# Optimization experiments

Hardware: AMD Instinct MI355X
Metric: run time of the kernel (lower is better)

The kernel has to match this reference:

```python
import jax, jax.numpy as jnp
import numpy as np

N_NODES = 50000
N_EDGES = 800000
N_GRAPHS = 2000
N_PAIRS = 4096
IN_CH = 64
EMB = 128
HID = 256
OUT = 1


def gcn_conv(x, edge_index, W, b):
    # PyG GCNConv: h = x @ W^T, then D^{-1/2}(A+I)D^{-1/2} h + b
    h = x @ W.T                                  # [N, out]
    row, col = edge_index[0], edge_index[1]
    ones = jnp.ones((edge_index.shape[1],), h.dtype)
    deg = jax.ops.segment_sum(ones, col, num_segments=N_NODES) + 1.0  # self-loop
    dinv = jax.lax.rsqrt(deg)
    norm = dinv[row] * dinv[col]                 # [E]
    agg = jax.ops.segment_sum(h[row] * norm[:, None], col, num_segments=N_NODES)
    agg = agg + h * (1.0 / deg)[:, None]         # self-loop term (dinv[i]^2)
    return agg + b


def setup_inputs() -> dict:
    key = jax.random.key(0)
    ks = jax.random.split(key, 10)
    x = jax.random.normal(ks[0], (N_NODES, IN_CH), jnp.float32)
    edge_index = jax.random.randint(ks[1], (2, N_EDGES), 0, N_NODES, jnp.int64)
    batch = jnp.sort(jax.random.randint(ks[2], (N_NODES,), 0, N_GRAPHS, jnp.int64))
    drug_drug_batch = jax.random.randint(ks[3], (2, N_PAIRS), 0, N_GRAPHS, jnp.int64)

    def xavier(k, shape):
        fan_out, fan_in = shape
        lim = jnp.sqrt(6.0 / (fan_in + fan_out))
        return jax.random.uniform(k, shape, jnp.float32, -lim, lim)

    return {
        "x": x, "edge_index": edge_index, "batch": batch,
        "drug_drug_batch": drug_drug_batch,
        "conv1_w": xavier(ks[4], (EMB, IN_CH)), "conv1_b": jnp.zeros((EMB,), jnp.float32),
        "conv2_w": xavier(ks[5], (EMB, EMB)), "conv2_b": jnp.zeros((EMB,), jnp.float32),
        "reg1_w": xavier(ks[6], (HID, 2 * EMB)), "reg1_b": jnp.zeros((HID,), jnp.float32),
        "reg2_w": xavier(ks[7], (OUT, HID)), "reg2_b": jnp.zeros((OUT,), jnp.float32),
    }


def reference(x, edge_index, batch, drug_drug_batch,
              conv1_w, conv1_b, conv2_w, conv2_b,
              reg1_w, reg1_b, reg2_w, reg2_b):
    h = jax.nn.relu(gcn_conv(x, edge_index, conv1_w, conv1_b))
    h = jax.nn.relu(gcn_conv(h, edge_index, conv2_w, conv2_b))

    # scatter_mean readout over graphs
    gsum = jax.ops.segment_sum(h, batch, num_segments=N_GRAPHS)
    cnt = jax.ops.segment_sum(jnp.ones((N_NODES,), h.dtype), batch, num_segments=N_GRAPHS)
    graph_embeds = gsum / jnp.maximum(cnt, 1.0)[:, None]

    # quantize drug ids to dense graph indices (np.digitize on unique+1, as in source)
    dd = np.asarray(drug_drug_batch)
    bins = np.unique(dd.flatten()) + 1
    q = jnp.asarray(np.digitize(dd, bins))       # [2, P]

    pairs = jnp.concatenate([graph_embeds[q[0]], graph_embeds[q[1]]], axis=1)  # [P, 2*EMB]
    out = jax.nn.relu(pairs @ reg1_w.T + reg1_b)
    return out @ reg2_w.T + reg2_b
```

## Files before the change

kernel.cpp:

```cpp
#include <hip/hip_runtime.h>

#define N_NODES  50000
#define N_PAD    50048
#define N_EDGES  800000
#define N_GRAPHS 2000
#define N_PAIRS  4096
#define IN_CH    64
#define EMB      128
#define HID      256
#define PPB      16
#define DPAD     16
#define GROB     1563

__device__ inline int wave_incl_scan(int x, int lane) {
    #pragma unroll
    for (int off = 1; off < 64; off <<= 1) {
        int y = __shfl_up(x, off, 64);
        if (lane >= off) x += y;
    }
    return x;
}

__global__ void k_zero(float4* __restrict__ p, int n4) {
    int i = blockIdx.x * 256 + threadIdx.x;
    if (i < n4) p[i] = make_float4(0.f, 0.f, 0.f, 0.f);
}

__global__ void k_pre(const int* __restrict__ col, const int* __restrict__ batch,
                      const float* __restrict__ w1, const float* __restrict__ w2,
                      int* __restrict__ deg, int* __restrict__ pos_e, int* __restrict__ cnt,
                      float* __restrict__ wt1, float* __restrict__ wt2,
                      const int* __restrict__ dd, int* __restrict__ rankx,
                      float4* __restrict__ gsum4) {
    int b = blockIdx.x, t = threadIdx.x;
    if (b < N_EDGES / 256) {
        int e = b * 256 + t;
        int c = col[e];
        pos_e[e] = atomicAdd(&deg[c * DPAD], 1);
        if (e < N_NODES) atomicAdd(&cnt[batch[e]], 1);
        if (e < EMB * IN_CH) {
            int j = e / IN_CH, k = e % IN_CH;
            wt1[k * EMB + j] = w1[e];
        } else if (e < EMB * IN_CH + EMB * EMB) {
            int q = e - EMB * IN_CH;
            int j = q / EMB, k = q % EMB;
            wt2[k * EMB + j] = w2[q];
        }
    } else if (b == N_EDGES / 256) {
        __shared__ int pres[N_GRAPHS];
        __shared__ int ws2[4];
        __shared__ int carry;
        int lane = t & 63, wid = t >> 6;
        for (int i = t; i < N_GRAPHS; i += 256) pres[i] = 0;
        __syncthreads();
        for (int i = t; i < 2 * N_PAIRS; i += 256) pres[dd[i]] = 1;
        if (t == 0) carry = 0;
        __syncthreads();
        for (int base = 0; base < N_GRAPHS; base += 256) {
            int i = base + t;
            int v = (i < N_GRAPHS) ? pres[i] : 0;
            int x = wave_incl_scan(v, lane);
            if (lane == 63) ws2[wid] = x;
            __syncthreads();
            int add = carry;
            for (int w = 0; w < wid; ++w) add += ws2[w];
            if (i < N_GRAPHS) rankx[i] = x - v + add;
            __syncthreads();
            if (t == 255) carry = add + x;
            __syncthreads();
        }
    } else {
        int i = (b - N_EDGES / 256 - 1) * 256 + t;
        for (int k = i; k < N_GRAPHS * EMB / 4; k += 4096)
            gsum4[k] = make_float4(0.f, 0.f, 0.f, 0.f);
    }
}

__global__ void k_scan1(const int* __restrict__ in, int* __restrict__ part, int n) {
    __shared__ int ws[4];
    int i = blockIdx.x * 256 + threadIdx.x;
    int lane = threadIdx.x & 63, wid = threadIdx.x >> 6;
    int v = (i < n) ? in[i * DPAD] : 0;
    int x = wave_incl_scan(v, lane);
    if (lane == 63) ws[wid] = x;
    __syncthreads();
    if (threadIdx.x == 0) part[blockIdx.x] = ws[0] + ws[1] + ws[2] + ws[3];
}

__global__ void k_scan3d(const int* __restrict__ in, const int* __restrict__ part,
                         int* __restrict__ off, float* __restrict__ dinv) {
    __shared__ int ws[4];
    __shared__ int psum[4];
    int t = threadIdx.x;
    int lane = t & 63, wid = t >> 6;
    int pp = 0;
    for (int w = t; w < (int)blockIdx.x; w += 256) pp += part[w];
    #pragma unroll
    for (int o = 32; o > 0; o >>= 1) pp += __shfl_down(pp, o, 64);
    if (lane == 0) psum[wid] = pp;
    int i = blockIdx.x * 256 + t;
    int v = (i < N_NODES) ? in[i * DPAD] : 0;
    int x = wave_incl_scan(v, lane);
    if (lane == 63) ws[wid] = x;
    __syncthreads();
    int add = psum[0] + psum[1] + psum[2] + psum[3];
    for (int w = 0; w < wid; ++w) add += ws[w];
    if (i < N_NODES) {
        off[i] = x - v + add;
        dinv[i] = 1.0f / sqrtf((float)(v + 1));
    }
    if (i == 0) off[N_NODES] = N_EDGES;
}

__global__ void k_fill_scale(const int* __restrict__ row, const int* __restrict__ col,
                             const int* __restrict__ pos_e, const int* __restrict__ off,
                             int* __restrict__ csr_row,
                             const float4* __restrict__ x, const float* __restrict__ dinv,
                             float4* __restrict__ xs) {
    int idx = blockIdx.x * 256 + threadIdx.x;
    if (idx < N_EDGES) {
        int c = col[idx];
        int p = pos_e[idx];
        csr_row[off[c] + p] = row[idx];
    } else {
        int i = idx - N_EDGES;
        int n = i >> 4;
        float d = dinv[n];
        float4 v = x[i];
        v.x *= d; v.y *= d; v.z *= d; v.w *= d;
        xs[i] = v;
    }
}

__device__ inline void f4add(float4& a, const float4 b) {
    a.x += b.x; a.y += b.y; a.z += b.z; a.w += b.w;
}

__global__ __launch_bounds__(256) void k_conv1f(
        const float4* __restrict__ xs, const int* __restrict__ csr_row,
        const int* __restrict__ off, const float* __restrict__ dinv,
        const float* __restrict__ w1t, const float* __restrict__ b1,
        float* __restrict__ h1s) {
    __shared__ __align__(16) float a_lds[32 * IN_CH];
    int t = threadIdx.x;
    int base = blockIdx.x * 32;
    {
        int c4l = t & 7;
        int nl = t >> 3;
        int n = base + nl;
        int s = 0, e = 0;
        float dn = 0.f;
        if (n < N_NODES) { s = off[n]; e = off[n + 1]; dn = dinv[n]; }
        #pragma unroll
        for (int g = 0; g < 2; ++g) {
            int c4 = c4l + g * 8;
            float4 acc = make_float4(0.f, 0.f, 0.f, 0.f);
            if (n < N_NODES) {
                acc = xs[n * 16 + c4];
                int i = s;
                for (; i + 8 <= e; i += 8) {
                    int r0 = csr_row[i + 0], r1 = csr_row[i + 1], r2 = csr_row[i + 2], r3 = csr_row[i + 3];
                    int r4 = csr_row[i + 4], r5 = csr_row[i + 5], r6 = csr_row[i + 6], r7 = csr_row[i + 7];
                    float4 a0 = xs[r0 * 16 + c4], a1 = xs[r1 * 16 + c4];
                    float4 a2 = xs[r2 * 16 + c4], a3 = xs[r3 * 16 + c4];
                    float4 a4 = xs[r4 * 16 + c4], a5 = xs[r5 * 16 + c4];
                    float4 a6 = xs[r6 * 16 + c4], a7 = xs[r7 * 16 + c4];
                    f4add(a0, a1); f4add(a2, a3); f4add(a4, a5); f4add(a6, a7);
                    f4add(a0, a2); f4add(a4, a6);
                    f4add(a0, a4);
                    f4add(acc, a0);
                }
                for (; i < e; ++i) {
                    float4 a = xs[csr_row[i] * 16 + c4];
                    f4add(acc, a);
                }
                acc.x *= dn; acc.y *= dn; acc.z *= dn; acc.w *= dn;
            }
            *reinterpret_cast<float4*>(&a_lds[nl * IN_CH + c4 * 4]) = acc;
        }
    }
    __syncthreads();
    {
        int cq = (t & 31) << 2;
        int rg = t >> 5;
        float4 acc[4];
        #pragma unroll
        for (int r = 0; r < 4; ++r) acc[r] = make_float4(0.f, 0.f, 0.f, 0.f);
        #pragma unroll 2
        for (int k = 0; k < IN_CH; k += 4) {
            float4 w0 = *reinterpret_cast<const float4*>(&w1t[(k + 0) * EMB + cq]);
            float4 w1 = *reinterpret_cast<const float4*>(&w1t[(k + 1) * EMB + cq]);
            float4 w2 = *reinterpret_cast<const float4*>(&w1t[(k + 2) * EMB + cq]);
            float4 w3 = *reinterpret_cast<const float4*>(&w1t[(k + 3) * EMB + cq]);
            #pragma unroll
            for (int r = 0; r < 4; ++r) {
                float4 a = *reinterpret_cast<const float4*>(&a_lds[(rg * 4 + r) * IN_CH + k]);
                acc[r].x = fmaf(a.x, w0.x, fmaf(a.y, w1.x, fmaf(a.z, w2.x, fmaf(a.w, w3.x, acc[r].x))));
                acc[r].y = fmaf(a.x, w0.y, fmaf(a.y, w1.y, fmaf(a.z, w2.y, fmaf(a.w, w3.y, acc[r].y))));
                acc[r].z = fmaf(a.x, w0.z, fmaf(a.y, w1.z, fmaf(a.z, w2.z, fmaf(a.w, w3.z, acc[r].z))));
                acc[r].w = fmaf(a.x, w0.w, fmaf(a.y, w1.w, fmaf(a.z, w2.w, fmaf(a.w, w3.w, acc[r].w))));
            }
        }
        float4 bv = *reinterpret_cast<const float4*>(&b1[cq]);
        #pragma unroll
        for (int r = 0; r < 4; ++r) {
            int row = base + rg * 4 + r;
            if (row < N_NODES) {
                float4 v = acc[r];
                v.x += bv.x; v.y += bv.y; v.z += bv.z; v.w += bv.w;
                float sc = dinv[row];
                v.x = fmaxf(v.x, 0.f) * sc; v.y = fmaxf(v.y, 0.f) * sc;
                v.z = fmaxf(v.z, 0.f) * sc; v.w = fmaxf(v.w, 0.f) * sc;
                *reinterpret_cast<float4*>(&h1s[(size_t)row * EMB + cq]) = v;
            }
        }
    }
}

template <int K>
__global__ void k_gemmv5(const float* __restrict__ A, const float* __restrict__ Wt,
                         float* __restrict__ out) {
    __shared__ __align__(16) float a_lds[64 * K];
    int t = threadIdx.x;
    {
        const float4* Ag = reinterpret_cast<const float4*>(A + (size_t)blockIdx.x * 64 * K);
        float4* Al = reinterpret_cast<float4*>(a_lds);
        constexpr int NV = (64 * K) / (4 * 256);
        #pragma unroll
        for (int i = 0; i < NV; ++i) Al[t + i * 256] = Ag[t + i * 256];
    }
    __syncthreads();
    int cq = (t & 31) << 2;
    int rg = t >> 5;
    float4 acc[8];
    #pragma unroll
    for (int r = 0; r < 8; ++r) acc[r] = make_float4(0.f, 0.f, 0.f, 0.f);
    #pragma unroll 2
    for (int k = 0; k < K; k += 4) {
        float4 w0 = *reinterpret_cast<const float4*>(&Wt[(k + 0) * EMB + cq]);
        float4 w1 = *reinterpret_cast<const float4*>(&Wt[(k + 1) * EMB + cq]);
        float4 w2 = *reinterpret_cast<const float4*>(&Wt[(k + 2) * EMB + cq]);
        float4 w3 = *reinterpret_cast<const float4*>(&Wt[(k + 3) * EMB + cq]);
        #pragma unroll
        for (int r = 0; r < 8; ++r) {
            float4 a = *reinterpret_cast<const float4*>(&a_lds[(rg * 8 + r) * K + k]);
            acc[r].x = fmaf(a.x, w0.x, fmaf(a.y, w1.x, fmaf(a.z, w2.x, fmaf(a.w, w3.x, acc[r].x))));
            acc[r].y = fmaf(a.x, w0.y, fmaf(a.y, w1.y, fmaf(a.z, w2.y, fmaf(a.w, w3.y, acc[r].y))));
            acc[r].z = fmaf(a.x, w0.z, fmaf(a.y, w1.z, fmaf(a.z, w2.z, fmaf(a.w, w3.z, acc[r].z))));
            acc[r].w = fmaf(a.x, w0.w, fmaf(a.y, w1.w, fmaf(a.z, w2.w, fmaf(a.w, w3.w, acc[r].w))));
        }
    }
    int row0 = blockIdx.x * 64 + rg * 8;
    #pragma unroll
    for (int r = 0; r < 8; ++r) {
        int row = row0 + r;
        if (row < N_NODES) {
            *reinterpret_cast<float4*>(&out[(size_t)row * EMB + cq]) = acc[r];
        }
    }
}

__global__ void k_gro(const float4* __restrict__ t2, const int* __restrict__ csr_row,
                      const int* __restrict__ off, const float* __restrict__ dinv,
                      const float* __restrict__ bias, const int* __restrict__ batch,
                      float* __restrict__ gsum) {
    __shared__ __align__(16) float hb[32][64];
    __shared__ int bg[32];
    int t = threadIdx.x;
    int bid = blockIdx.x;
    int half = (bid >= GROB) ? 1 : 0;
    int n0 = (half ? bid - GROB : bid) * 32;
    int local = t >> 3;
    int c4l = t & 7;
    int n = n0 + local;
    if (t < 32) bg[t] = (n0 + t < N_NODES) ? batch[n0 + t] : -1;
    int s = 0, e = 0;
    float dn = 0.f;
    bool valid = (n < N_NODES);
    if (valid) { s = off[n]; e = off[n + 1]; dn = dinv[n]; }
    #pragma unroll
    for (int g = 0; g < 2; ++g) {
        int cidx = half * 16 + g * 8 + c4l;
        float4 acc = make_float4(0.f, 0.f, 0.f, 0.f);
        if (valid) {
            acc = t2[(size_t)n * 32 + cidx];
            int i = s;
            for (; i + 8 <= e; i += 8) {
                int r0 = csr_row[i + 0], r1 = csr_row[i + 1], r2 = csr_row[i + 2], r3 = csr_row[i + 3];
                int r4 = csr_row[i + 4], r5 = csr_row[i + 5], r6 = csr_row[i + 6], r7 = csr_row[i + 7];
                float4 a0 = t2[(size_t)r0 * 32 + cidx], a1 = t2[(size_t)r1 * 32 + cidx];
                float4 a2 = t2[(size_t)r2 * 32 + cidx], a3 = t2[(size_t)r3 * 32 + cidx];
                float4 a4 = t2[(size_t)r4 * 32 + cidx], a5 = t2[(size_t)r5 * 32 + cidx];
                float4 a6 = t2[(size_t)r6 * 32 + cidx], a7 = t2[(size_t)r7 * 32 + cidx];
                f4add(a0, a1); f4add(a2, a3); f4add(a4, a5); f4add(a6, a7);
                f4add(a0, a2); f4add(a4, a6);
                f4add(a0, a4);
                f4add(acc, a0);
            }
            for (; i < e; ++i) {
                float4 a = t2[(size_t)csr_row[i] * 32 + cidx];
                f4add(acc, a);
            }
            float4 b = reinterpret_cast<const float4*>(bias)[cidx];
            acc.x = fmaxf(fmaf(acc.x, dn, b.x), 0.f);
            acc.y = fmaxf(fmaf(acc.y, dn, b.y), 0.f);
            acc.z = fmaxf(fmaf(acc.z, dn, b.z), 0.f);
            acc.w = fmaxf(fmaf(acc.w, dn, b.w), 0.f);
        }
        *reinterpret_cast<float4*>(&hb[local][(g * 8 + c4l) * 4]) = acc;
    }
    __syncthreads();
    {
        int ch = t & 63, q = t >> 6;
        int j0 = q * 8;
        int g = bg[j0];
        if (g >= 0) {
            float a = 0.f;
            #pragma unroll
            for (int j = j0; j < j0 + 8; ++j) {
                int gj = bg[j];
                if (gj < 0) break;
                if (gj != g) { atomicAdd(&gsum[g * EMB + half * 64 + ch], a); a = 0.f; g = gj; }
                a += hb[j][ch];
            }
            atomicAdd(&gsum[g * EMB + half * 64 + ch], a);
        }
    }
}

__global__ void k_mlp16(const float* __restrict__ gemb, const int* __restrict__ cnt,
                        const int* __restrict__ dd, const int* __restrict__ rankx,
                        const float* __restrict__ w1, const float* __restrict__ b1,
                        const float* __restrict__ w2, const float* __restrict__ b2,
                        float* __restrict__ out) {
    __shared__ __align__(16) float pv[PPB][2 * EMB];
    __shared__ float wpart[4][PPB];
    int p0 = blockIdx.x * PPB;
    int t = threadIdx.x;
    int lane = t & 63, wid = t >> 6;
    #pragma unroll
    for (int j = 0; j < PPB; ++j) {
        int p = p0 + j;
        if (t < EMB) {
            int ga = rankx[dd[p]];
            int ca = cnt[ga];
            float ra = 1.0f / (float)(ca > 1 ? ca : 1);
            pv[j][t] = gemb[ga * EMB + t] * ra;
        } else {
            int gb = rankx[dd[N_PAIRS + p]];
            int cb = cnt[gb];
            float rb = 1.0f / (float)(cb > 1 ? cb : 1);
            pv[j][t] = gemb[gb * EMB + (t - EMB)] * rb;
        }
    }
    __syncthreads();
    float acc[PPB];
    float bv = b1[t];
    #pragma unroll
    for (int j = 0; j < PPB; ++j) acc[j] = bv;
    const float4* wrow = reinterpret_cast<const float4*>(&w1[t * 2 * EMB]);
    for (int k = 0; k < (2 * EMB) / 4; ++k) {
        float4 w = wrow[k];
        #pragma unroll
        for (int j = 0; j < PPB; ++j) {
            const float4 xv = *reinterpret_cast<const float4*>(&pv[j][k * 4]);
            acc[j] = fmaf(xv.x, w.x, fmaf(xv.y, w.y, fmaf(xv.z, w.z, fmaf(xv.w, w.w, acc[j]))));
        }
    }
    float w2t = w2[t];
    float contrib[PPB];
    #pragma unroll
    for (int j = 0; j < PPB; ++j) contrib[j] = fmaxf(acc[j], 0.f) * w2t;
    #pragma unroll
    for (int off = 32; off > 0; off >>= 1) {
        #pragma unroll
        for (int j = 0; j < PPB; ++j) contrib[j] += __shfl_down(contrib[j], off, 64);
    }
    if (lane == 0) {
        #pragma unroll
        for (int j = 0; j < PPB; ++j) wpart[wid][j] = contrib[j];
    }
    __syncthreads();
    if (t < PPB) {
        out[p0 + t] = wpart[0][t] + wpart[1][t] + wpart[2][t] + wpart[3][t] + b2[0];
    }
}

extern "C" void kernel_launch(void* const* d_in, const int* in_sizes, int n_in,
                              void* d_out, int out_size, void* d_ws, size_t ws_size,
                              hipStream_t stream) {
    const float* x        = (const float*)d_in[0];
    const int*   ei       = (const int*)d_in[1];
    const int*   batch    = (const int*)d_in[2];
    const int*   dd       = (const int*)d_in[3];
    const float* conv1_w  = (const float*)d_in[4];
    const float* conv1_b  = (const float*)d_in[5];
    const float* conv2_w  = (const float*)d_in[6];
    const float* conv2_b  = (const float*)d_in[7];
    const float* reg1_w   = (const float*)d_in[8];
    const float* reg1_b   = (const float*)d_in[9];
    const float* reg2_w   = (const float*)d_in[10];
    const float* reg2_b   = (const float*)d_in[11];
    float* outp = (float*)d_out;

    const int* ei_row = ei;
    const int* ei_col = ei + N_EDGES;

    char* ws = (char*)d_ws;
    size_t o = 0;
    auto alloc = [&](size_t bytes) -> void* {
        void* p = ws + o;
        o = (o + bytes + 255) & ~(size_t)255;
        return p;
    };
    size_t zero_start = o;
    int*   deg     = (int*)alloc((size_t)N_NODES * DPAD * 4);
    int*   cnt     = (int*)alloc(N_GRAPHS * 4);
    size_t zero_bytes = o - zero_start;
    float* gsum    = (float*)alloc(N_GRAPHS * EMB * 4);
    int*   off     = (int*)alloc((N_NODES + 1) * 4);
    float* dinv    = (float*)alloc(N_NODES * 4);
    int*   part    = (int*)alloc(256 * 4);
    int*   pos_e   = (int*)alloc(N_EDGES * 4);
    int*   csr_row = (int*)alloc(N_EDGES * 4);
    int*   rankx   = (int*)alloc(N_GRAPHS * 4);
    float* Wt1     = (float*)alloc(IN_CH * EMB * 4);
    float* Wt2     = (float*)alloc(EMB * EMB * 4);
    float* h1s     = (float*)alloc((size_t)N_PAD * EMB * 4);
    float* t2      = (float*)alloc((size_t)N_PAD * EMB * 4);
    float* xs      = t2;

    (void)ws_size; (void)in_sizes; (void)n_in; (void)out_size;

    {
        int n4 = (int)(zero_bytes / 16);
        k_zero<<<(n4 + 255) / 256, 256, 0, stream>>>((float4*)(ws + zero_start), n4);
    }

    k_pre<<<N_EDGES / 256 + 1 + 16, 256, 0, stream>>>(ei_col, batch, conv1_w, conv2_w,
                                                      deg, pos_e, cnt, Wt1, Wt2,
                                                      dd, rankx, (float4*)gsum);
    {
        int nb = (N_NODES + 255) / 256;
        k_scan1<<<nb, 256, 0, stream>>>(deg, part, N_NODES);
        k_scan3d<<<nb, 256, 0, stream>>>(deg, part, off, dinv);
    }
    k_fill_scale<<<(N_EDGES + N_NODES * (IN_CH / 4)) / 256, 256, 0, stream>>>(
        ei_row, ei_col, pos_e, off, csr_row, (const float4*)x, dinv, (float4*)xs);

    k_conv1f<<<N_PAD / 32, 256, 0, stream>>>(
        (const float4*)xs, csr_row, off, dinv, Wt1, conv1_b, h1s);

    k_gemmv5<EMB><<<N_PAD / 64, 256, 0, stream>>>(h1s, Wt2, t2);
    k_gro<<<2 * GROB, 256, 0, stream>>>(
        (const float4*)t2, csr_row, off, dinv, conv2_b, batch, gsum);

    k_mlp16<<<N_PAIRS / PPB, 256, 0, stream>>>(gsum, cnt, dd, rankx,
                                               reg1_w, reg1_b, reg2_w, reg2_b, outp);
}
```

Baseline: 216.3 us.

## Replace CSR prefix scan with fixed-stride per-node edge buckets

Drops the two degree-scan kernels and the offset array. Each node now gets a fixed 64-slot bucket in csr_row, indexed as node*64 + position, and degree and dinv are computed inside the fill/scale kernel. k_gro is also retiled to 64 nodes per block with a padded shared buffer and longer per-wave graph runs for the atomics. The aim is to cut launch and scan overhead. The cost is a larger, sparser csr_row footprint, and the code silently assumes no node has more than 64 incoming edges.

```diff
diff --git a/kernel.cpp b/kernel.cpp
--- a/kernel.cpp
+++ b/kernel.cpp
@@ -10,7 +10,8 @@
 #define HID      256
 #define PPB      16
 #define DPAD     16
-#define GROB     1563
+#define CSTRIDE  64
+#define GROB64   782
 
 __device__ inline int wave_incl_scan(int x, int lane) {
     #pragma unroll
@@ -76,56 +77,21 @@
     }
 }
 
-__global__ void k_scan1(const int* __restrict__ in, int* __restrict__ part, int n) {
-    __shared__ int ws[4];
-    int i = blockIdx.x * 256 + threadIdx.x;
-    int lane = threadIdx.x & 63, wid = threadIdx.x >> 6;
-    int v = (i < n) ? in[i * DPAD] : 0;
-    int x = wave_incl_scan(v, lane);
-    if (lane == 63) ws[wid] = x;
-    __syncthreads();
-    if (threadIdx.x == 0) part[blockIdx.x] = ws[0] + ws[1] + ws[2] + ws[3];
-}
-
-__global__ void k_scan3d(const int* __restrict__ in, const int* __restrict__ part,
-                         int* __restrict__ off, float* __restrict__ dinv) {
-    __shared__ int ws[4];
-    __shared__ int psum[4];
-    int t = threadIdx.x;
-    int lane = t & 63, wid = t >> 6;
-    int pp = 0;
-    for (int w = t; w < (int)blockIdx.x; w += 256) pp += part[w];
-    #pragma unroll
-    for (int o = 32; o > 0; o >>= 1) pp += __shfl_down(pp, o, 64);
-    if (lane == 0) psum[wid] = pp;
-    int i = blockIdx.x * 256 + t;
-    int v = (i < N_NODES) ? in[i * DPAD] : 0;
-    int x = wave_incl_scan(v, lane);
-    if (lane == 63) ws[wid] = x;
-    __syncthreads();
-    int add = psum[0] + psum[1] + psum[2] + psum[3];
-    for (int w = 0; w < wid; ++w) add += ws[w];
-    if (i < N_NODES) {
-        off[i] = x - v + add;
-        dinv[i] = 1.0f / sqrtf((float)(v + 1));
-    }
-    if (i == 0) off[N_NODES] = N_EDGES;
-}
-
 __global__ void k_fill_scale(const int* __restrict__ row, const int* __restrict__ col,
-                             const int* __restrict__ pos_e, const int* __restrict__ off,
+                             const int* __restrict__ pos_e, const int* __restrict__ deg,
                              int* __restrict__ csr_row,
-                             const float4* __restrict__ x, const float* __restrict__ dinv,
-                             float4* __restrict__ xs) {
+                             const float4* __restrict__ x, float* __restrict__ dinv,
+                             int* __restrict__ degc, float4* __restrict__ xs) {
     int idx = blockIdx.x * 256 + threadIdx.x;
     if (idx < N_EDGES) {
         int c = col[idx];
-        int p = pos_e[idx];
-        csr_row[off[c] + p] = row[idx];
+        csr_row[c * CSTRIDE + pos_e[idx]] = row[idx];
     } else {
         int i = idx - N_EDGES;
         int n = i >> 4;
-        float d = dinv[n];
+        int dg = deg[n * DPAD];
+        float d = 1.0f / sqrtf((float)(dg + 1));
+        if ((i & 15) == 0) { dinv[n] = d; degc[n] = dg; }
         float4 v = x[i];
         v.x *= d; v.y *= d; v.z *= d; v.w *= d;
         xs[i] = v;
@@ -138,7 +104,7 @@
 
 __global__ __launch_bounds__(256) void k_conv1f(
         const float4* __restrict__ xs, const int* __restrict__ csr_row,
-        const int* __restrict__ off, const float* __restrict__ dinv,
+        const int* __restrict__ degc, const float* __restrict__ dinv,
         const float* __restrict__ w1t, const float* __restrict__ b1,
         float* __restrict__ h1s) {
     __shared__ __align__(16) float a_lds[32 * IN_CH];
@@ -148,9 +114,9 @@
         int c4l = t & 7;
         int nl = t >> 3;
         int n = base + nl;
-        int s = 0, e = 0;
+        int s = n * CSTRIDE, e = s;
         float dn = 0.f;
-        if (n < N_NODES) { s = off[n]; e = off[n + 1]; dn = dinv[n]; }
+        if (n < N_NODES) { e = s + degc[n]; dn = dinv[n]; }
         #pragma unroll
         for (int g = 0; g < 2; ++g) {
             int c4 = c4l + g * 8;
@@ -261,26 +227,26 @@
 }
 
 __global__ void k_gro(const float4* __restrict__ t2, const int* __restrict__ csr_row,
-                      const int* __restrict__ off, const float* __restrict__ dinv,
+                      const int* __restrict__ degc, const float* __restrict__ dinv,
                       const float* __restrict__ bias, const int* __restrict__ batch,
                       float* __restrict__ gsum) {
-    __shared__ __align__(16) float hb[32][64];
-    __shared__ int bg[32];
+    __shared__ float hb[64][68];
+    __shared__ int bg[64];
     int t = threadIdx.x;
     int bid = blockIdx.x;
-    int half = (bid >= GROB) ? 1 : 0;
-    int n0 = (half ? bid - GROB : bid) * 32;
-    int local = t >> 3;
-    int c4l = t & 7;
+    int half = (bid >= GROB64) ? 1 : 0;
+    int n0 = (half ? bid - GROB64 : bid) * 64;
+    int local = t >> 2;
+    int c4l = t & 3;
     int n = n0 + local;
-    if (t < 32) bg[t] = (n0 + t < N_NODES) ? batch[n0 + t] : -1;
-    int s = 0, e = 0;
+    if (t < 64) bg[t] = (n0 + t < N_NODES) ? batch[n0 + t] : -1;
+    int s = n * CSTRIDE, e = s;
     float dn = 0.f;
     bool valid = (n < N_NODES);
-    if (valid) { s = off[n]; e = off[n + 1]; dn = dinv[n]; }
-    #pragma unroll
-    for (int g = 0; g < 2; ++g) {
-        int cidx = half * 16 + g * 8 + c4l;
+    if (valid) { e = s + degc[n]; dn = dinv[n]; }
+    #pragma unroll
+    for (int g = 0; g < 4; ++g) {
+        int cidx = half * 16 + g * 4 + c4l;
         float4 acc = make_float4(0.f, 0.f, 0.f, 0.f);
         if (valid) {
             acc = t2[(size_t)n * 32 + cidx];
@@ -307,17 +273,19 @@
             acc.z = fmaxf(fmaf(acc.z, dn, b.z), 0.f);
             acc.w = fmaxf(fmaf(acc.w, dn, b.w), 0.f);
         }
-        *reinterpret_cast<float4*>(&hb[local][(g * 8 + c4l) * 4]) = acc;
+        int cb = (g * 4 + c4l) * 4;
+        hb[local][cb + 0] = acc.x; hb[local][cb + 1] = acc.y;
+        hb[local][cb + 2] = acc.z; hb[local][cb + 3] = acc.w;
     }
     __syncthreads();
     {
         int ch = t & 63, q = t >> 6;
-        int j0 = q * 8;
+        int j0 = q * 16;
         int g = bg[j0];
         if (g >= 0) {
             float a = 0.f;
-            #pragma unroll
-            for (int j = j0; j < j0 + 8; ++j) {
+            #pragma unroll 4
+            for (int j = j0; j < j0 + 16; ++j) {
                 int gj = bg[j];
                 if (gj < 0) break;
                 if (gj != g) { atomicAdd(&gsum[g * EMB + half * 64 + ch], a); a = 0.f; g = gj; }
@@ -418,11 +386,10 @@
     int*   cnt     = (int*)alloc(N_GRAPHS * 4);
     size_t zero_bytes = o - zero_start;
     float* gsum    = (float*)alloc(N_GRAPHS * EMB * 4);
-    int*   off     = (int*)alloc((N_NODES + 1) * 4);
     float* dinv    = (float*)alloc(N_NODES * 4);
-    int*   part    = (int*)alloc(256 * 4);
+    int*   degc    = (int*)alloc(N_NODES * 4);
     int*   pos_e   = (int*)alloc(N_EDGES * 4);
-    int*   csr_row = (int*)alloc(N_EDGES * 4);
+    int*   csr_row = (int*)alloc((size_t)N_PAD * CSTRIDE * 4);
     int*   rankx   = (int*)alloc(N_GRAPHS * 4);
     float* Wt1     = (float*)alloc(IN_CH * EMB * 4);
     float* Wt2     = (float*)alloc(EMB * EMB * 4);
@@ -440,20 +407,16 @@
     k_pre<<<N_EDGES / 256 + 1 + 16, 256, 0, stream>>>(ei_col, batch, conv1_w, conv2_w,
                                                       deg, pos_e, cnt, Wt1, Wt2,
                                                       dd, rankx, (float4*)gsum);
-    {
-        int nb = (N_NODES + 255) / 256;
-        k_scan1<<<nb, 256, 0, stream>>>(deg, part, N_NODES);
-        k_scan3d<<<nb, 256, 0, stream>>>(deg, part, off, dinv);
-    }
+
     k_fill_scale<<<(N_EDGES + N_NODES * (IN_CH / 4)) / 256, 256, 0, stream>>>(
-        ei_row, ei_col, pos_e, off, csr_row, (const float4*)x, dinv, (float4*)xs);
+        ei_row, ei_col, pos_e, deg, csr_row, (const float4*)x, dinv, degc, (float4*)xs);
 
     k_conv1f<<<N_PAD / 32, 256, 0, stream>>>(
-        (const float4*)xs, csr_row, off, dinv, Wt1, conv1_b, h1s);
+        (const float4*)xs, csr_row, degc, dinv, Wt1, conv1_b, h1s);
 
     k_gemmv5<EMB><<<N_PAD / 64, 256, 0, stream>>>(h1s, Wt2, t2);
-    k_gro<<<2 * GROB, 256, 0, stream>>>(
-        (const float4*)t2, csr_row, off, dinv, conv2_b, batch, gsum);
+    k_gro<<<2 * GROB64, 256, 0, stream>>>(
+        (const float4*)t2, csr_row, degc, dinv, conv2_b, batch, gsum);
 
     k_mlp16<<<N_PAIRS / PPB, 256, 0, stream>>>(gsum, cnt, dd, rankx,
                                                reg1_w, reg1_b, reg2_w, reg2_b, outp);
```

Result: slower. 270.9 us (+25.3%).
